# Kernel tuning notes

Hardware: AMD Instinct MI355X
Metric: run time of the kernel (lower is better)

## Reference

```python
import jax, jax.numpy as jnp
import numpy as np

# ---- static config (severity=3 -> params (0.4, 1, 1)) ----
B, C, H, W = 64, 3, 224, 224
SIGMA = 0.4
MAX_DELTA = 1
ITERATIONS = 1
RADIUS = int(4.0 * SIGMA + 0.5)  # scipy/skimage default truncate=4.0 -> radius 2
_x = np.arange(-RADIUS, RADIUS + 1, dtype=np.float64)
_k = np.exp(-0.5 * (_x / SIGMA) ** 2)
KERNEL = jnp.asarray(_k / _k.sum(), dtype=jnp.float32)  # 5 taps

# swap coordinate order: y = H-1..1 (outer), x = W-1..1 (inner), repeated ITERATIONS times
_ys = np.arange(H - MAX_DELTA, MAX_DELTA - 1, -1, dtype=np.int32)
_xs = np.arange(W - MAX_DELTA, MAX_DELTA - 1, -1, dtype=np.int32)
YS = jnp.asarray(np.tile(np.repeat(_ys, _xs.size), ITERATIONS))  # [ITER*N]
XS = jnp.asarray(np.tile(np.tile(_xs, _ys.size), ITERATIONS))    # [ITER*N]
N_SWAPS = YS.shape[0]


def _gaussian_blur(img):
    """Separable Gaussian, mode='nearest' (edge pad), img [B,H,W,C] float."""
    p = jnp.pad(img, ((0, 0), (RADIUS, RADIUS), (0, 0), (0, 0)), mode='edge')
    img = sum(KERNEL[i] * p[:, i:i + H] for i in range(2 * RADIUS + 1))
    p = jnp.pad(img, ((0, 0), (0, 0), (RADIUS, RADIUS), (0, 0)), mode='edge')
    img = sum(KERNEL[i] * p[:, :, i:i + W] for i in range(2 * RADIUS + 1))
    return img


def _swap_single(img, d):
    """Sequential random pixel swaps. img [H,W,C]; d [N_SWAPS,2] in {-1,0,1}."""
    def body(im, t):
        y, x, dy, dx = t
        yp = jnp.clip(y + dy, 0, H - 1)
        xp = jnp.clip(x + dx, 0, W - 1)
        a = im[y, x]
        b = im[yp, xp]
        # set order matches original temp-swap (self-swap is identity)
        im = im.at[y, x].set(b).at[yp, xp].set(a)
        return im, None
    im, _ = jax.lax.scan(body, img, (YS, XS, d[:, 0], d[:, 1]))
    return im


def setup_inputs() -> dict:
    key = jax.random.key(0)
    k1, k2 = jax.random.split(key)
    x = jax.random.uniform(k1, (B, C, H, W), dtype=jnp.float32)
    deltas = jax.random.randint(k2, (B, N_SWAPS, 2), 0, 3, dtype=jnp.int32)
    return {"x": x, "deltas": deltas}


def reference(x, deltas):
    # tensor_to_numpy_uint8: clamp(x*255) then byte() (truncation)
    img = jnp.floor(jnp.clip(x * 255.0, 0.0, 255.0))        # [B,C,H,W], uint8 values
    img = jnp.transpose(img, (0, 2, 3, 1))                   # [B,H,W,C]
    # first blur + np.uint8 cast (truncation)
    img = jnp.floor(_gaussian_blur(img / 255.0) * 255.0)
    # sequential random pixel swaps, per image
    d = deltas - 1                                           # values in {-1,0,1}
    img = jax.vmap(_swap_single)(img, d)
    # second blur, clip, uint8 cast, then /255 back to float tensor
    img = _gaussian_blur(img / 255.0)
    img = jnp.floor(jnp.clip(img * 255.0, 0.0, 255.0)) / 255.0
    return jnp.transpose(img, (0, 3, 1, 2))                  # [B,C,H,W]
```

## Files before the change

### kernel.cpp

```cpp
#include <hip/hip_runtime.h>
#include <hip/hip_bf16.h>

#define KW0 0.91921792f
#define KW1 0.04038762f
#define KW2 3.42560e-6f

#define HH 224
#define WW 224
#define NSW 49729
#define LEAF_SLOT 676
#define LEAF_IMG 150748
#define P_STRIDE 50176

__global__ __launch_bounds__(256) void prep_kernel(const float* __restrict__ x,
                                                   const int* __restrict__ deltas,
                                                   unsigned char* __restrict__ img,
                                                   unsigned short* __restrict__ leafG) {
    __shared__ __align__(16) unsigned char smem[46976];
    const int bid = blockIdx.x;
    const int tid = threadIdx.x;

    if (bid < 448) {
        const int j = bid % 7;
        const int b = bid / 7;
        const int U = j * 32;
        unsigned short* smA = (unsigned short*)smem;
        unsigned* pk = (unsigned*)(smem + 43264);
        const int u = U + tid;

        {
            const int2* Dbase = (const int2*)deltas + (size_t)b * NSW + (size_t)U * 223;
            for (int w = tid; w < 32 * 28; w += 256) {
                const int r = w / 28, k = w - r * 28;
                if (U + r < 223) {
                    const int base = r * 223 + 8 * k;
                    unsigned word = 0;
#pragma unroll
                    for (int jj = 0; jj < 8; ++jj) {
                        const int i = 8 * k + jj;
                        unsigned idx = 5u;
                        if (i < 223) {
                            int2 d = Dbase[base + jj];
                            unsigned px = (unsigned)d.x, py = (unsigned)d.y;
                            if (U + r == 0) px = min(px, 1u);
                            if (i == 0) py = min(py, 1u);
                            idx = px * 4u + py;
                        }
                        word |= idx << (4 * jj);
                    }
                    pk[r * 29 + k] = word;
                }
            }
        }
        __syncthreads();

        if (tid < 32 && u < 223) {
            const int y = 223 - u;
            const unsigned b0r = (unsigned)(y - 1) << 8;
            const unsigned b1r = (unsigned)y << 8;
            const unsigned b2r = (unsigned)(y + 1) << 8;
            unsigned short* Lf = &smA[tid * LEAF_SLOT];
            const unsigned* pkr = &pk[tid * 29];

            unsigned w00 = b0r + 222, w01 = b0r + 223, w02 = b0r + 224;
            unsigned w10 = b1r + 222, w11 = b1r + 223, w12 = b1r + 224;
            unsigned w20 = b2r + 222, w21 = b2r + 223, w22 = b2r + 224;

            unsigned wA_ = pkr[0], wB_ = pkr[1], wC_ = pkr[2];

#define GB_STEP(KK, CA, CB, CC) {                                               \
            const int x_ = 223 - (ibase + (KK));                                \
            const unsigned wsel_ = (((KK) >> 3) == 0) ? wA_                     \
                                 : ((((KK) >> 3) == 1) ? wB_ : wC_);            \
            const unsigned idx_ = (wsel_ >> (4 * ((KK) & 7))) & 15u;            \
            const unsigned pr_ = idx_ >> 2, pc_ = idx_ & 3u;                    \
            const bool pc0_ = (pc_ == 0u), pc1_ = (pc_ == 1u);                  \
            const bool pr0_ = (pr_ == 0u), pr1_ = (pr_ == 1u);                  \
            const unsigned s0_ = pc0_ ? w0##CA : (pc1_ ? w0##CB : w0##CC);      \
            const unsigned s1_ = pc0_ ? w1##CA : (pc1_ ? w1##CB : w1##CC);      \
            const unsigned s2_ = pc0_ ? w2##CA : (pc1_ ? w2##CB : w2##CC);      \
            const unsigned v_ = pr0_ ? s0_ : (pr1_ ? s1_ : s2_);                \
            const unsigned c_ = w1##CB;                                         \
            w0##CA = idx_ == 0u  ? c_ : w0##CA;                                 \
            w0##CB = idx_ == 1u  ? c_ : w0##CB;                                 \
            w0##CC = idx_ == 2u  ? c_ : w0##CC;                                 \
            w1##CA = idx_ == 4u  ? c_ : w1##CA;                                 \
            w1##CC = idx_ == 6u  ? c_ : w1##CC;                                 \
            w2##CA = idx_ == 8u  ? c_ : w2##CA;                                 \
            w2##CB = idx_ == 9u  ? c_ : w2##CB;                                 \
            w2##CC = idx_ == 10u ? c_ : w2##CC;                                 \
            w1##CB = v_;                                                        \
            Lf[x_ + 1]   = (unsigned short)w0##CC;                              \
            Lf[x_ + 225] = (unsigned short)w1##CC;                              \
            Lf[x_ + 449] = (unsigned short)w2##CC;                              \
            w0##CC = b0r + (unsigned)(x_ - 2);                                  \
            w1##CC = b1r + (unsigned)(x_ - 2);                                  \
            w2##CC = b2r + (unsigned)(x_ - 2);                                  \
        }
#define GB_TRIPLE(K0) GB_STEP((K0), 0, 1, 2) GB_STEP((K0)+1, 2, 0, 1) GB_STEP((K0)+2, 1, 2, 0)
            for (int blk = 0; blk < 9; ++blk) {
                const int ibase = 24 * blk;
                const unsigned nA_ = pkr[min(3 * blk + 3, 27)];
                const unsigned nB_ = pkr[min(3 * blk + 4, 27)];
                const unsigned nC_ = pkr[min(3 * blk + 5, 27)];
                GB_TRIPLE(0)  GB_TRIPLE(3)  GB_TRIPLE(6)  GB_TRIPLE(9)
                GB_TRIPLE(12) GB_TRIPLE(15) GB_TRIPLE(18) GB_TRIPLE(21)
                wA_ = nA_; wB_ = nB_; wC_ = nC_;
            }
            {
                const int ibase = 216;
                GB_TRIPLE(0) GB_TRIPLE(3) GB_STEP(6, 0, 1, 2)
            }
            Lf[1] = (unsigned short)w01; Lf[225] = (unsigned short)w11; Lf[449] = (unsigned short)w21;
            Lf[0] = (unsigned short)w00; Lf[224] = (unsigned short)w10; Lf[448] = (unsigned short)w20;
#undef GB_TRIPLE
#undef GB_STEP
        }
        __syncthreads();

        const int nuT = min(32, 223 - U);
        uint2* dst = (uint2*)(leafG + (size_t)b * LEAF_IMG + (size_t)U * LEAF_SLOT);
        const uint2* srcp = (const uint2*)smA;
        for (int l = tid; l < nuT * (LEAF_SLOT / 4); l += 256) dst[l] = srcp[l];
    } else {
        const int k = bid - 448;
        const int rb = k % 28;
        const int c = (k / 28) % 3;
        const int b = k / 84;
        const int y0 = rb * 8;
        float* A = (float*)smem;
        float* Bv = A + 12 * WW;
        const float* xp = x + ((size_t)(b * 3 + c)) * HH * WW;

        for (int l = tid; l < 12 * WW; l += 256) {
            int r = l / WW, xx = l - r * WW;
            int gy = min(max(y0 + r - 2, 0), HH - 1);
            float v = xp[gy * WW + xx];
            v = floorf(fminf(fmaxf(v * 255.0f, 0.0f), 255.0f));
            A[r * WW + xx] = v;
        }
        __syncthreads();
        for (int l = tid; l < 8 * WW; l += 256) {
            int r = l / WW, xx = l - r * WW;
            Bv[r * WW + xx] = KW2 * A[r * WW + xx] + KW1 * A[(r + 1) * WW + xx]
                            + KW0 * A[(r + 2) * WW + xx] + KW1 * A[(r + 3) * WW + xx]
                            + KW2 * A[(r + 4) * WW + xx];
        }
        __syncthreads();
        unsigned char* op = img + ((size_t)(b * 3 + c)) * HH * WW;
        for (int l = tid; l < 8 * WW; l += 256) {
            int r = l / WW, xx = l - r * WW;
            int c0 = max(xx - 2, 0), c1 = max(xx - 1, 0);
            int c3 = min(xx + 1, WW - 1), c4 = min(xx + 2, WW - 1);
            float s = KW2 * Bv[r * WW + c0] + KW1 * Bv[r * WW + c1] + KW0 * Bv[r * WW + xx]
                    + KW1 * Bv[r * WW + c3] + KW2 * Bv[r * WW + c4];
            op[(y0 + r) * WW + xx] = (unsigned char)floorf(s);
        }
    }
}

__global__ __launch_bounds__(256) void chaseP_kernel(const unsigned short* __restrict__ leafG,
                                                     unsigned short* __restrict__ P) {
    const int b = blockIdx.y;
    const int base = blockIdx.x * 2048;
    const unsigned short* L = leafG + (size_t)b * LEAF_IMG;
    unsigned short* Pb = P + (size_t)b * P_STRIDE;
    const int e0 = base + (int)threadIdx.x * 8;
    if (e0 >= P_STRIDE) return;

    unsigned rv[8], cv[8]; bool done[8]; int us[8];
    const int pr0 = e0 / 224, pc0 = e0 - pr0 * 224;
    int umax = -1;
#pragma unroll
    for (int t = 0; t < 8; ++t) {
        const int pc = pc0 + t;
        const int pr = pr0 + (pc >= 224 ? 1 : 0);
        rv[t] = (unsigned)pr;
        cv[t] = (unsigned)(pc >= 224 ? pc - 224 : pc);
        us[t] = min(222, 224 - pr);
        done[t] = false;
        umax = max(umax, us[t]);
    }
    for (int u = umax; u >= 0; --u) {
        const unsigned short* Lu = L + u * LEAF_SLOT;
        const int bot = 222 - u;
        bool all = true;
#pragma unroll
        for (int t = 0; t < 8; ++t) {
            if (!done[t] && u <= us[t]) {
                if ((int)rv[t] < bot) done[t] = true;
                else {
                    const unsigned q = Lu[__mul24((int)rv[t] - bot, 224) + (int)cv[t]];
                    rv[t] = q >> 8;
                    cv[t] = q & 255u;
                }
            }
            all = all && done[t];
        }
        if (all) break;
    }
    unsigned res[8];
#pragma unroll
    for (int t = 0; t < 8; ++t)
        res[t] = (unsigned)(__mul24((int)rv[t], 224) + (int)cv[t]);
    uint4 v;
    v.x = res[0] | (res[1] << 16);
    v.y = res[2] | (res[3] << 16);
    v.z = res[4] | (res[5] << 16);
    v.w = res[6] | (res[7] << 16);
    *(uint4*)(Pb + e0) = v;
}

__global__ __launch_bounds__(256) void apply_kernel(unsigned char* __restrict__ img,
                                                    const unsigned short* __restrict__ P) {
    const int plane = blockIdx.x;
    const int b = plane / 3;
    __shared__ __align__(16) unsigned char im[HH * WW];
    unsigned char* g = img + (size_t)plane * (HH * WW);
    for (int l = threadIdx.x; l < (HH * WW) / 16; l += 256)
        ((int4*)im)[l] = ((const int4*)g)[l];
    __syncthreads();
    const unsigned short* Pp = P + (size_t)b * P_STRIDE;
    for (int t = threadIdx.x; t < (HH * WW) / 8; t += 256) {
        uint4 pe = ((const uint4*)Pp)[t];
        unsigned e0 = pe.x & 0xffffu, e1 = pe.x >> 16;
        unsigned e2 = pe.y & 0xffffu, e3 = pe.y >> 16;
        unsigned e4 = pe.z & 0xffffu, e5 = pe.z >> 16;
        unsigned e6 = pe.w & 0xffffu, e7 = pe.w >> 16;
        unsigned lo = (unsigned)im[e0] | ((unsigned)im[e1] << 8)
                    | ((unsigned)im[e2] << 16) | ((unsigned)im[e3] << 24);
        unsigned hi = (unsigned)im[e4] | ((unsigned)im[e5] << 8)
                    | ((unsigned)im[e6] << 16) | ((unsigned)im[e7] << 24);
        ((uint2*)g)[t] = make_uint2(lo, hi);
    }
}

__global__ __launch_bounds__(256) void blur2_kernel(const unsigned char* __restrict__ img,
                                                    float* __restrict__ out) {
    const int rb = blockIdx.x, c = blockIdx.y, b = blockIdx.z;
    const int y0 = rb * 8;
    __shared__ float A[12][WW];
    __shared__ float Bv[8][WW];
    const unsigned char* ip = img + ((size_t)(b * 3 + c)) * HH * WW;

    for (int l = threadIdx.x; l < 12 * WW; l += 256) {
        int r = l / WW, xx = l - r * WW;
        int gy = min(max(y0 + r - 2, 0), HH - 1);
        A[r][xx] = (float)ip[gy * WW + xx];
    }
    __syncthreads();
    for (int l = threadIdx.x; l < 8 * WW; l += 256) {
        int r = l / WW, xx = l - r * WW;
        Bv[r][xx] = KW2 * A[r][xx] + KW1 * A[r + 1][xx] + KW0 * A[r + 2][xx]
                  + KW1 * A[r + 3][xx] + KW2 * A[r + 4][xx];
    }
    __syncthreads();
    float* op = out + ((size_t)(b * 3 + c)) * HH * WW;
    for (int l = threadIdx.x; l < 8 * WW; l += 256) {
        int r = l / WW, xx = l - r * WW;
        int c0 = max(xx - 2, 0), c1 = max(xx - 1, 0);
        int c3 = min(xx + 1, WW - 1), c4 = min(xx + 2, WW - 1);
        float s = KW2 * Bv[r][c0] + KW1 * Bv[r][c1] + KW0 * Bv[r][xx]
                + KW1 * Bv[r][c3] + KW2 * Bv[r][c4];
        s = fminf(fmaxf(s, 0.0f), 255.0f);
        op[(y0 + r) * WW + xx] = floorf(s) / 255.0f;
    }
}

__global__ __launch_bounds__(256) void blur2_apply_kernel(const unsigned char* __restrict__ img,
                                                          const unsigned short* __restrict__ P,
                                                          float* __restrict__ out) {
    const int rb = blockIdx.x, c = blockIdx.y, b = blockIdx.z;
    const int y0 = rb * 8;
    __shared__ float A[12][WW];
    __shared__ float Bv[8][WW];
    const unsigned char* ip = img + ((size_t)(b * 3 + c)) * HH * WW;
    const unsigned short* Pp = P + (size_t)b * P_STRIDE;

    for (int l = threadIdx.x; l < 12 * WW; l += 256) {
        int r = l / WW, xx = l - r * WW;
        int gy = min(max(y0 + r - 2, 0), HH - 1);
        unsigned q = Pp[gy * WW + xx];
        A[r][xx] = (float)ip[q];
    }
    __syncthreads();
    for (int l = threadIdx.x; l < 8 * WW; l += 256) {
        int r = l / WW, xx = l - r * WW;
        Bv[r][xx] = KW2 * A[r][xx] + KW1 * A[r + 1][xx] + KW0 * A[r + 2][xx]
                  + KW1 * A[r + 3][xx] + KW2 * A[r + 4][xx];
    }
    __syncthreads();
    float* op = out + ((size_t)(b * 3 + c)) * HH * WW;
    for (int l = threadIdx.x; l < 8 * WW; l += 256) {
        int r = l / WW, xx = l - r * WW;
        int c0 = max(xx - 2, 0), c1 = max(xx - 1, 0);
        int c3 = min(xx + 1, WW - 1), c4 = min(xx + 2, WW - 1);
        float s = KW2 * Bv[r][c0] + KW1 * Bv[r][c1] + KW0 * Bv[r][xx]
                + KW1 * Bv[r][c3] + KW2 * Bv[r][c4];
        s = fminf(fmaxf(s, 0.0f), 255.0f);
        op[(y0 + r) * WW + xx] = floorf(s) / 255.0f;
    }
}

extern "C" void kernel_launch(void* const* d_in, const int* in_sizes, int n_in,
                              void* d_out, int out_size, void* d_ws, size_t ws_size,
                              hipStream_t stream) {
    const float* x      = (const float*)d_in[0];
    const int*   deltas = (const int*)d_in[1];
    float*       out    = (float*)d_out;
    unsigned char* img  = (unsigned char*)d_ws;

    unsigned short* leafG = (unsigned short*)d_out;
    unsigned short* pFall = leafG + (size_t)64 * LEAF_IMG;

    const bool fused = ws_size >= (size_t)9633792 + (size_t)64 * P_STRIDE * 2;
    unsigned short* P = fused ? (unsigned short*)(img + 9633792) : pFall;

    prep_kernel<<<dim3(448 + 5376), 256, 0, stream>>>(x, deltas, img, leafG);
    chaseP_kernel<<<dim3(25, 64), 256, 0, stream>>>(leafG, P);

    dim3 gb(28, 3, 64);
    if (fused) {
        blur2_apply_kernel<<<gb, 256, 0, stream>>>(img, P, out);
    } else {
        apply_kernel<<<dim3(192), 256, 0, stream>>>(img, P);
        blur2_kernel<<<gb, 256, 0, stream>>>(img, out);
    }
}
```

Before: 133.6 us.

## Split fused prep kernel into separate leaf-build and first-blur kernels

Splits the heterogeneous prep kernel, whose blocks branched into either swap-leaf construction or the first blur, into two kernels: build_kernel and blur1_kernel. Each now gets its own grid and shared-memory footprint, so the lightweight blur blocks no longer reserve the large leaf buffer. The blur input load is also vectorised to float4. The cost is an extra launch and serialisation on one stream: the serial, 32-thread build work can no longer overlap with the blur blocks.

```diff
diff --git a/kernel.cpp b/kernel.cpp
--- a/kernel.cpp
+++ b/kernel.cpp
@@ -12,61 +12,57 @@
 #define LEAF_IMG 150748
 #define P_STRIDE 50176
 
-__global__ __launch_bounds__(256) void prep_kernel(const float* __restrict__ x,
-                                                   const int* __restrict__ deltas,
-                                                   unsigned char* __restrict__ img,
-                                                   unsigned short* __restrict__ leafG) {
-    __shared__ __align__(16) unsigned char smem[46976];
-    const int bid = blockIdx.x;
+__global__ __launch_bounds__(256) void build_kernel(const int* __restrict__ deltas,
+                                                    unsigned short* __restrict__ leafG) {
+    const int j = blockIdx.x;
+    const int b = blockIdx.y;
+    const int U = j * 32;
+
+    __shared__ __align__(16) unsigned short smA[32 * LEAF_SLOT];
+    __shared__ unsigned pk[32 * 29];
+
     const int tid = threadIdx.x;
-
-    if (bid < 448) {
-        const int j = bid % 7;
-        const int b = bid / 7;
-        const int U = j * 32;
-        unsigned short* smA = (unsigned short*)smem;
-        unsigned* pk = (unsigned*)(smem + 43264);
-        const int u = U + tid;
-
-        {
-            const int2* Dbase = (const int2*)deltas + (size_t)b * NSW + (size_t)U * 223;
-            for (int w = tid; w < 32 * 28; w += 256) {
-                const int r = w / 28, k = w - r * 28;
-                if (U + r < 223) {
-                    const int base = r * 223 + 8 * k;
-                    unsigned word = 0;
+    const int u = U + tid;
+
+    {
+        const int2* Dbase = (const int2*)deltas + (size_t)b * NSW + (size_t)U * 223;
+        for (int w = tid; w < 32 * 28; w += 256) {
+            const int r = w / 28, k = w - r * 28;
+            if (U + r < 223) {
+                const int base = r * 223 + 8 * k;
+                unsigned word = 0;
 #pragma unroll
-                    for (int jj = 0; jj < 8; ++jj) {
-                        const int i = 8 * k + jj;
-                        unsigned idx = 5u;
-                        if (i < 223) {
-                            int2 d = Dbase[base + jj];
-                            unsigned px = (unsigned)d.x, py = (unsigned)d.y;
-                            if (U + r == 0) px = min(px, 1u);
-                            if (i == 0) py = min(py, 1u);
-                            idx = px * 4u + py;
-                        }
-                        word |= idx << (4 * jj);
+                for (int jj = 0; jj < 8; ++jj) {
+                    const int i = 8 * k + jj;
+                    unsigned idx = 5u;
+                    if (i < 223) {
+                        int2 d = Dbase[base + jj];
+                        unsigned px = (unsigned)d.x, py = (unsigned)d.y;
+                        if (U + r == 0) px = min(px, 1u);
+                        if (i == 0) py = min(py, 1u);
+                        idx = px * 4u + py;
                     }
-                    pk[r * 29 + k] = word;
+                    word |= idx << (4 * jj);
                 }
+                pk[r * 29 + k] = word;
             }
         }
-        __syncthreads();
-
-        if (tid < 32 && u < 223) {
-            const int y = 223 - u;
-            const unsigned b0r = (unsigned)(y - 1) << 8;
-            const unsigned b1r = (unsigned)y << 8;
-            const unsigned b2r = (unsigned)(y + 1) << 8;
-            unsigned short* Lf = &smA[tid * LEAF_SLOT];
-            const unsigned* pkr = &pk[tid * 29];
-
-            unsigned w00 = b0r + 222, w01 = b0r + 223, w02 = b0r + 224;
-            unsigned w10 = b1r + 222, w11 = b1r + 223, w12 = b1r + 224;
-            unsigned w20 = b2r + 222, w21 = b2r + 223, w22 = b2r + 224;
-
-            unsigned wA_ = pkr[0], wB_ = pkr[1], wC_ = pkr[2];
+    }
+    __syncthreads();
+
+    if (tid < 32 && u < 223) {
+        const int y = 223 - u;
+        const unsigned b0r = (unsigned)(y - 1) << 8;
+        const unsigned b1r = (unsigned)y << 8;
+        const unsigned b2r = (unsigned)(y + 1) << 8;
+        unsigned short* Lf = &smA[tid * LEAF_SLOT];
+        const unsigned* pkr = &pk[tid * 29];
+
+        unsigned w00 = b0r + 222, w01 = b0r + 223, w02 = b0r + 224;
+        unsigned w10 = b1r + 222, w11 = b1r + 223, w12 = b1r + 224;
+        unsigned w20 = b2r + 222, w21 = b2r + 223, w22 = b2r + 224;
+
+        unsigned wA_ = pkr[0], wB_ = pkr[1], wC_ = pkr[2];
 
 #define GB_STEP(KK, CA, CB, CC) {                                               \
             const int x_ = 223 - (ibase + (KK));                                \
@@ -98,64 +94,64 @@
             w2##CC = b2r + (unsigned)(x_ - 2);                                  \
         }
 #define GB_TRIPLE(K0) GB_STEP((K0), 0, 1, 2) GB_STEP((K0)+1, 2, 0, 1) GB_STEP((K0)+2, 1, 2, 0)
-            for (int blk = 0; blk < 9; ++blk) {
-                const int ibase = 24 * blk;
-                const unsigned nA_ = pkr[min(3 * blk + 3, 27)];
-                const unsigned nB_ = pkr[min(3 * blk + 4, 27)];
-                const unsigned nC_ = pkr[min(3 * blk + 5, 27)];
-                GB_TRIPLE(0)  GB_TRIPLE(3)  GB_TRIPLE(6)  GB_TRIPLE(9)
-                GB_TRIPLE(12) GB_TRIPLE(15) GB_TRIPLE(18) GB_TRIPLE(21)
-                wA_ = nA_; wB_ = nB_; wC_ = nC_;
-            }
-            {
-                const int ibase = 216;
-                GB_TRIPLE(0) GB_TRIPLE(3) GB_STEP(6, 0, 1, 2)
-            }
-            Lf[1] = (unsigned short)w01; Lf[225] = (unsigned short)w11; Lf[449] = (unsigned short)w21;
-            Lf[0] = (unsigned short)w00; Lf[224] = (unsigned short)w10; Lf[448] = (unsigned short)w20;
+        for (int blk = 0; blk < 9; ++blk) {
+            const int ibase = 24 * blk;
+            const unsigned nA_ = pkr[min(3 * blk + 3, 27)];
+            const unsigned nB_ = pkr[min(3 * blk + 4, 27)];
+            const unsigned nC_ = pkr[min(3 * blk + 5, 27)];
+            GB_TRIPLE(0)  GB_TRIPLE(3)  GB_TRIPLE(6)  GB_TRIPLE(9)
+            GB_TRIPLE(12) GB_TRIPLE(15) GB_TRIPLE(18) GB_TRIPLE(21)
+            wA_ = nA_; wB_ = nB_; wC_ = nC_;
+        }
+        {
+            const int ibase = 216;
+            GB_TRIPLE(0) GB_TRIPLE(3) GB_STEP(6, 0, 1, 2)
+        }
+        Lf[1] = (unsigned short)w01; Lf[225] = (unsigned short)w11; Lf[449] = (unsigned short)w21;
+        Lf[0] = (unsigned short)w00; Lf[224] = (unsigned short)w10; Lf[448] = (unsigned short)w20;
 #undef GB_TRIPLE
 #undef GB_STEP
-        }
-        __syncthreads();
-
-        const int nuT = min(32, 223 - U);
-        uint2* dst = (uint2*)(leafG + (size_t)b * LEAF_IMG + (size_t)U * LEAF_SLOT);
-        const uint2* srcp = (const uint2*)smA;
-        for (int l = tid; l < nuT * (LEAF_SLOT / 4); l += 256) dst[l] = srcp[l];
-    } else {
-        const int k = bid - 448;
-        const int rb = k % 28;
-        const int c = (k / 28) % 3;
-        const int b = k / 84;
-        const int y0 = rb * 8;
-        float* A = (float*)smem;
-        float* Bv = A + 12 * WW;
-        const float* xp = x + ((size_t)(b * 3 + c)) * HH * WW;
-
-        for (int l = tid; l < 12 * WW; l += 256) {
-            int r = l / WW, xx = l - r * WW;
-            int gy = min(max(y0 + r - 2, 0), HH - 1);
-            float v = xp[gy * WW + xx];
-            v = floorf(fminf(fmaxf(v * 255.0f, 0.0f), 255.0f));
-            A[r * WW + xx] = v;
-        }
-        __syncthreads();
-        for (int l = tid; l < 8 * WW; l += 256) {
-            int r = l / WW, xx = l - r * WW;
-            Bv[r * WW + xx] = KW2 * A[r * WW + xx] + KW1 * A[(r + 1) * WW + xx]
-                            + KW0 * A[(r + 2) * WW + xx] + KW1 * A[(r + 3) * WW + xx]
-                            + KW2 * A[(r + 4) * WW + xx];
-        }
-        __syncthreads();
-        unsigned char* op = img + ((size_t)(b * 3 + c)) * HH * WW;
-        for (int l = tid; l < 8 * WW; l += 256) {
-            int r = l / WW, xx = l - r * WW;
-            int c0 = max(xx - 2, 0), c1 = max(xx - 1, 0);
-            int c3 = min(xx + 1, WW - 1), c4 = min(xx + 2, WW - 1);
-            float s = KW2 * Bv[r * WW + c0] + KW1 * Bv[r * WW + c1] + KW0 * Bv[r * WW + xx]
-                    + KW1 * Bv[r * WW + c3] + KW2 * Bv[r * WW + c4];
-            op[(y0 + r) * WW + xx] = (unsigned char)floorf(s);
-        }
+    }
+    __syncthreads();
+
+    const int nuT = min(32, 223 - U);
+    uint2* dst = (uint2*)(leafG + (size_t)b * LEAF_IMG + (size_t)U * LEAF_SLOT);
+    const uint2* srcp = (const uint2*)smA;
+    for (int l = tid; l < nuT * (LEAF_SLOT / 4); l += 256) dst[l] = srcp[l];
+}
+
+__global__ __launch_bounds__(256) void blur1_kernel(const float* __restrict__ x,
+                                                    unsigned char* __restrict__ img) {
+    const int rb = blockIdx.x, c = blockIdx.y, b = blockIdx.z;
+    const int y0 = rb * 8;
+    __shared__ float A[12][WW];
+    __shared__ float Bv[8][WW];
+    const float* xp = x + ((size_t)(b * 3 + c)) * HH * WW;
+
+    for (int l = threadIdx.x; l < 12 * 56; l += 256) {
+        int r = l / 56, k4 = (l - r * 56) * 4;
+        int gy = min(max(y0 + r - 2, 0), HH - 1);
+        float4 v = *(const float4*)(xp + gy * WW + k4);
+        A[r][k4]     = floorf(fminf(fmaxf(v.x * 255.0f, 0.0f), 255.0f));
+        A[r][k4 + 1] = floorf(fminf(fmaxf(v.y * 255.0f, 0.0f), 255.0f));
+        A[r][k4 + 2] = floorf(fminf(fmaxf(v.z * 255.0f, 0.0f), 255.0f));
+        A[r][k4 + 3] = floorf(fminf(fmaxf(v.w * 255.0f, 0.0f), 255.0f));
+    }
+    __syncthreads();
+    for (int l = threadIdx.x; l < 8 * WW; l += 256) {
+        int r = l / WW, xx = l - r * WW;
+        Bv[r][xx] = KW2 * A[r][xx] + KW1 * A[r + 1][xx] + KW0 * A[r + 2][xx]
+                  + KW1 * A[r + 3][xx] + KW2 * A[r + 4][xx];
+    }
+    __syncthreads();
+    unsigned char* op = img + ((size_t)(b * 3 + c)) * HH * WW;
+    for (int l = threadIdx.x; l < 8 * WW; l += 256) {
+        int r = l / WW, xx = l - r * WW;
+        int c0 = max(xx - 2, 0), c1 = max(xx - 1, 0);
+        int c3 = min(xx + 1, WW - 1), c4 = min(xx + 2, WW - 1);
+        float s = KW2 * Bv[r][c0] + KW1 * Bv[r][c1] + KW0 * Bv[r][xx]
+                + KW1 * Bv[r][c3] + KW2 * Bv[r][c4];
+        op[(y0 + r) * WW + xx] = (unsigned char)floorf(s);
     }
 }
 
@@ -316,7 +312,8 @@
     const bool fused = ws_size >= (size_t)9633792 + (size_t)64 * P_STRIDE * 2;
     unsigned short* P = fused ? (unsigned short*)(img + 9633792) : pFall;
 
-    prep_kernel<<<dim3(448 + 5376), 256, 0, stream>>>(x, deltas, img, leafG);
+    build_kernel<<<dim3(7, 64), 256, 0, stream>>>(deltas, leafG);
+    blur1_kernel<<<dim3(28, 3, 64), 256, 0, stream>>>(x, img);
     chaseP_kernel<<<dim3(25, 64), 256, 0, stream>>>(leafG, P);
 
     dim3 gb(28, 3, 64);
```

Result: faster. 120.5 us (-9.8%).
